# Kernel tuning notes

Measured on AMD Instinct MI355X. Metric: run time of the kernel, lower is better.

The kernel has to match this reference:

```python
import jax, jax.numpy as jnp
import numpy as np

B, T, C, H = 1, 1024, 2048, 32
N = C // H  # head_dim = 64
EPS_GN = 0.00064


def setup_inputs() -> dict:
    key = jax.random.key(0)
    ks = jax.random.split(key, 40)
    f32 = jnp.float32

    def rn(k, shape, s):
        return jax.random.normal(k, shape, f32) * s

    layer_idx, n_layer = 12, 24
    r01 = layer_idx / (n_layer - 1)
    r1a0 = 1.0 - layer_idx / n_layer
    ddd = (jnp.arange(C, dtype=f32) / C).reshape(1, 1, C)
    decay_speed = -7.0 + 5.0 * (jnp.arange(C, dtype=f32) / (C - 1)) ** (0.85 + r01 ** 0.5)

    inp = dict(
        hidden_states=jax.random.normal(ks[0], (B, T, C), f32),
        Wq=rn(ks[1], (C, C), 0.02), Wk=rn(ks[2], (C, C), 0.02),
        Wv=rn(ks[3], (C, C), 0.02), Wo=rn(ks[4], (C, C), 0.02),
        time_maa_x=1.0 - ddd ** (0.6 * r1a0 ** 0.9),
        time_maa_rg=rn(ks[5], (1, 1, C), 0.01),
        time_maa_wa=rn(ks[6], (1, 1, C), 0.01),
        time_maa_k=rn(ks[7], (1, 1, C), 0.01),
        time_maa_v=rn(ks[8], (1, 1, C), 0.01),
        time_maa_w1=rn(ks[9], (C, 4 * 32), 0.01),
        time_maa_w2=rn(ks[10], (4, 32, C), 0.01),
        time_decay=decay_speed.reshape(1, 1, C) + 0.5,
        time_decay_w1=rn(ks[11], (C, 64), 0.01),
        time_decay_w2=rn(ks[12], (64, C), 0.01),
        time_aaaaa=rn(ks[13], (1, 1, C), 0.01),
        time_aaa_w1=rn(ks[14], (C, 16), 0.01),
        time_aaa_w2=rn(ks[15], (16, C), 0.01),
        time_kkk_w1=rn(ks[16], (C, 16), 0.01),
        time_kkk_w2=rn(ks[17], (16, C), 0.01),
        gate_w1=rn(ks[18], (C, 128), 0.01),
        gate_w2=rn(ks[19], (128, C), 0.01),
        time_misc_a=rn(ks[20], (1, 1, C), 0.01),
        ma_w1=rn(ks[21], (C, 16), 0.01),
        ma_w2=rn(ks[22], (16, C), 0.01),
        time_misc_k=rn(ks[23], (1, 1, C), 0.01),
        mk_w1=rn(ks[24], (C, 16), 0.01),
        mk_w2=rn(ks[25], (16, C), 0.01),
        time_faaaa=rn(ks[26], (1, 1, H, N), 0.01),
        ln_w=1.0 + rn(ks[27], (C,), 0.01),
        ln_b=rn(ks[28], (C,), 0.01),
    )
    return inp


def _wkv7(r, w, k, v, a, b):
    """RWKV7 matrix-state recurrence. Inputs [B,T,C]; per head state [N,N].
    state_t = state * exp(w_t) (per key-col) + (state @ a_t) b_t^T + v_t k_t^T;
    out_t = state_t @ r_t."""
    hs = lambda x: x.reshape(B, T, H, N)
    r, k, v, a, b = map(hs, (r, k, v, a, b))
    dec = jnp.exp(hs(w))  # w <= -0.5, decay in (0,1)

    def step(state, inp):
        r_t, d_t, k_t, v_t, a_t, b_t = inp  # each [B,H,N]
        sa = jnp.einsum('bhij,bhj->bhi', state, a_t)
        state = (state * d_t[:, :, None, :]
                 + sa[..., None] * b_t[:, :, None, :]
                 + v_t[..., None] * k_t[:, :, None, :])
        out = jnp.einsum('bhij,bhj->bhi', state, r_t)
        return state, out

    xs = tuple(jnp.moveaxis(t, 1, 0) for t in (r, dec, k, v, a, b))  # [T,B,H,N]
    state0 = jnp.zeros((B, H, N, N), r.dtype)
    _, out = jax.lax.scan(step, state0, xs)
    return jnp.moveaxis(out, 0, 1).reshape(B, T, C)


def _group_norm(x, w, b):
    xg = x.reshape(B, T, H, N)
    mu = xg.mean(-1, keepdims=True)
    var = xg.var(-1, keepdims=True)
    xn = (xg - mu) * jax.lax.rsqrt(var + EPS_GN)
    return xn.reshape(B, T, C) * w + b


def reference(hidden_states, Wq, Wk, Wv, Wo, time_maa_x, time_maa_rg, time_maa_wa,
              time_maa_k, time_maa_v, time_maa_w1, time_maa_w2, time_decay,
              time_decay_w1, time_decay_w2, time_aaaaa, time_aaa_w1, time_aaa_w2,
              time_kkk_w1, time_kkk_w2, gate_w1, gate_w2, time_misc_a, ma_w1, ma_w2,
              time_misc_k, mk_w1, mk_w2, time_faaaa, ln_w, ln_b):
    x = hidden_states  # T already multiple of 16, so no padding branch
    dxprev = jnp.pad(x, ((0, 0), (1, 0), (0, 0)))[:, :-1] - x  # token shift
    xxx = x + dxprev * time_maa_x
    mix = jnp.tanh(xxx @ time_maa_w1).reshape(B, T, 4, 32)
    mix = jnp.einsum('btfd,fdc->fbtc', mix, time_maa_w2)  # [4,B,T,C]
    mrg, mwa, mk_mix, mv = mix[0], mix[1], mix[2], mix[3]
    xrg = x + dxprev * (time_maa_rg + mrg)
    xwa = x + dxprev * (time_maa_wa + mwa)
    xk = x + dxprev * (time_maa_k + mk_mix)
    xv = x + dxprev * (time_maa_v + mv)

    r = xrg @ Wq
    w = -jax.nn.softplus(-(time_decay + jnp.tanh(xwa @ time_decay_w1) @ time_decay_w2)) - 0.5
    k = xk @ Wk
    v = xv @ Wv
    g = jnp.tanh(xrg @ gate_w1) @ gate_w2

    kk = k + jnp.tanh(xk @ time_kkk_w1) @ time_kkk_w2
    kkh = kk.reshape(B, T, H, N)
    kk = (kkh / jnp.maximum(jnp.linalg.norm(kkh, axis=-1, keepdims=True), 1e-12)).reshape(B, T, C)

    a = jax.nn.sigmoid(time_aaaaa + (xwa @ time_aaa_w1) @ time_aaa_w2)
    ma = jax.nn.sigmoid(time_misc_a + (xwa @ ma_w1) @ ma_w2)
    k = k * ma + k * a * (1.0 - ma)
    mk_g = jax.nn.sigmoid(time_misc_k + (xk @ mk_w1) @ mk_w2)
    k = k * jnp.exp(jnp.minimum(w * mk_g, 0.0))

    y = _wkv7(r, w, k, v, -kk, kk * a)
    y = _group_norm(y, ln_w, ln_b)
    rh, kh, vh = (t.reshape(B, T, H, N) for t in (r, k, v))
    y = y + ((rh * kh * time_faaaa).sum(-1, keepdims=True) * vh).reshape(B, T, C)
    return (y * g) @ Wo
```

## Files before the change

### kernel.cpp

```cpp
#include <hip/hip_runtime.h>


#define T_ 1024
#define C_ 2048
#define H_ 32
#define N_ 64

using half8  = __attribute__((ext_vector_type(8))) _Float16;
using half4  = __attribute__((ext_vector_type(4))) _Float16;
using floatx4 = __attribute__((ext_vector_type(4))) float;

#define DPP_ADD(v, ctrl) \
    ((v) + __int_as_float(__builtin_amdgcn_update_dpp( \
        0, __float_as_int(v), (ctrl), 0xf, 0xf, true)))
#define REDUCE16(v) do { \
    v = DPP_ADD(v, 0xB1); v = DPP_ADD(v, 0x4E); \
    v = DPP_ADD(v, 0x141); v = DPP_ADD(v, 0x140); } while (0)

__device__ __forceinline__ void async_cp16(const void* g, void* l) {
    __builtin_amdgcn_global_load_lds(
        (const __attribute__((address_space(1))) void*)g,
        (__attribute__((address_space(3))) void*)l, 16, 0, 0);
}

__global__ __launch_bounds__(256) void k_tr(
    const float* __restrict__ W0, const float* __restrict__ W1,
    const float* __restrict__ W2, const float* __restrict__ W3,
    _Float16* __restrict__ D0, _Float16* __restrict__ D1,
    _Float16* __restrict__ D2, _Float16* __restrict__ D3)
{
    const int z = blockIdx.z;
    const float* S = (z == 0) ? W0 : (z == 1) ? W1 : (z == 2) ? W2 : W3;
    _Float16* D = (z == 0) ? D0 : (z == 1) ? D1 : (z == 2) ? D2 : D3;
    const int nb = blockIdx.x * 64, kb = blockIdx.y * 64;
    __shared__ __align__(16) float tile[64][65];
    const int tr = threadIdx.x >> 4, tc4 = (threadIdx.x & 15) * 4;
#pragma unroll
    for (int p = 0; p < 4; ++p) {
        int row = p * 16 + tr;
        float4 v = *(const float4*)&S[(size_t)(kb + row) * C_ + nb + tc4];
        tile[row][tc4 + 0] = v.x; tile[row][tc4 + 1] = v.y;
        tile[row][tc4 + 2] = v.z; tile[row][tc4 + 3] = v.w;
    }
    __syncthreads();
#pragma unroll
    for (int p = 0; p < 4; ++p) {
        int n = p * 16 + tr;
        half4 u;
        u[0] = (_Float16)tile[tc4 + 0][n];
        u[1] = (_Float16)tile[tc4 + 1][n];
        u[2] = (_Float16)tile[tc4 + 2][n];
        u[3] = (_Float16)tile[tc4 + 3][n];
        *(half4*)&D[(size_t)(nb + n) * C_ + kb + tc4] = u;
    }
}

__global__ __launch_bounds__(256) void k_trW(
    const float* __restrict__ maa_w1, const float* __restrict__ gate_w1,
    const float* __restrict__ decay_w1, const float* __restrict__ aaa_w1,
    const float* __restrict__ ma_w1, const float* __restrict__ kkk_w1,
    const float* __restrict__ mk_w1,
    _Float16* __restrict__ WTm, _Float16* __restrict__ WTl)
{
    const int z = blockIdx.z;
    const int k = blockIdx.x * 256 + threadIdx.x;
    const int n = blockIdx.y;
    if (z == 0 && n >= 128) return;
    const float* src; int stride, col;
    _Float16* dst;
    if (z == 0) { src = maa_w1; stride = 128; col = n; dst = WTm; }
    else {
        dst = WTl;
        if (n < 128)      { src = gate_w1;  stride = 128; col = n; }
        else if (n < 192) { src = decay_w1; stride = 64;  col = n - 128; }
        else if (n < 208) { src = aaa_w1;   stride = 16;  col = n - 192; }
        else if (n < 224) { src = ma_w1;    stride = 16;  col = n - 208; }
        else if (n < 240) { src = kkk_w1;   stride = 16;  col = n - 224; }
        else              { src = mk_w1;    stride = 16;  col = n - 240; }
    }
    dst[(size_t)n * C_ + k] = (_Float16)src[(size_t)k * stride + col];
}

__global__ __launch_bounds__(256) void k_prep(
    const float* __restrict__ X, const float* __restrict__ maa_x,
    _Float16* __restrict__ xxxH)
{
    const size_t idx = (size_t)blockIdx.x * 256 + threadIdx.x;
    const int c = (int)(idx & (C_ - 1));
    float cur = X[idx];
    float prev = (idx >= C_) ? X[idx - C_] : 0.0f;
    xxxH[idx] = (_Float16)(cur + (prev - cur) * maa_x[c]);
}

__global__ __launch_bounds__(256) void k_lora(
    int which,
    const _Float16* __restrict__ Axxx, const _Float16* __restrict__ Axrg,
    const _Float16* __restrict__ Axwa, const _Float16* __restrict__ Axk,
    const _Float16* __restrict__ WTm, const _Float16* __restrict__ WTl,
    float* __restrict__ m1p, float* __restrict__ l2p)
{
    const int mt = blockIdx.x;
    const int nt = blockIdx.y;
    const int ks = blockIdx.z;
    const _Float16* A; const _Float16* BT; float* O; int ostride;
    if (which == 0) { A = Axxx; BT = WTm; O = m1p; ostride = 128; }
    else {
        BT = WTl; O = l2p; ostride = 256;
        A = (nt < 4) ? Axrg : (nt < 7) ? Axwa : Axk;
    }
    O += (size_t)ks * T_ * ostride;
    const int m0 = mt * 64, n0 = nt * 32, k0 = ks * 512;
    const int tid = threadIdx.x;
    __shared__ __align__(16) _Float16 As[64 * 40];
    __shared__ __align__(16) _Float16 Bs[32 * 40];
    const int lane = tid & 63, wv = tid >> 6;
    const int r16 = lane & 15, q = lane >> 4;

    floatx4 acc[2];
    { floatx4 zv = {0.f, 0.f, 0.f, 0.f}; acc[0] = zv; acc[1] = zv; }

    const int arow = tid >> 2, ac8 = (tid & 3) * 8;
    const _Float16* ag = A + (size_t)(m0 + arow) * C_ + k0 + ac8;
    const _Float16* bg = BT + (size_t)(n0 + (tid >> 2)) * C_ + k0 + ac8;

    for (int kc = 0; kc < 512; kc += 32) {
        half8 av = *(const half8*)(ag + kc);
        half8 bv;
        if (tid < 128) bv = *(const half8*)(bg + kc);
        *(half8*)&As[arow * 40 + ac8] = av;
        if (tid < 128) *(half8*)&Bs[(tid >> 2) * 40 + ac8] = bv;
        __syncthreads();
        half8 af = *(const half8*)&As[(wv * 16 + r16) * 40 + q * 8];
        half8 b0 = *(const half8*)&Bs[(r16) * 40 + q * 8];
        half8 b1 = *(const half8*)&Bs[(16 + r16) * 40 + q * 8];
        acc[0] = __builtin_amdgcn_mfma_f32_16x16x32_f16(af, b0, acc[0], 0, 0, 0);
        acc[1] = __builtin_amdgcn_mfma_f32_16x16x32_f16(af, b1, acc[1], 0, 0, 0);
        __syncthreads();
    }
#pragma unroll
    for (int j = 0; j < 2; ++j)
#pragma unroll
        for (int e = 0; e < 4; ++e) {
            int row = m0 + wv * 16 + q * 4 + e;
            int col = n0 + j * 16 + r16;
            O[(size_t)row * ostride + col] = acc[j][e];
        }
}

__global__ __launch_bounds__(256) void k_xmix(
    const float* __restrict__ X, const float* __restrict__ m1p,
    const float* __restrict__ w2,
    const float* __restrict__ mrg, const float* __restrict__ mwa,
    const float* __restrict__ mk, const float* __restrict__ mv,
    _Float16* __restrict__ xrgH, _Float16* __restrict__ xwaH,
    _Float16* __restrict__ xkH, _Float16* __restrict__ xvH)
{
    const int tid = threadIdx.x;
    const int c = blockIdx.x * 256 + tid;
    const int t0 = blockIdx.y * 16;
    const size_t P = (size_t)T_ * 128;
    __shared__ __align__(16) float m1s[16][128];
#pragma unroll
    for (int p = 0; p < 2; ++p) {
        int id = tid + p * 256;
        int r = id >> 5, c4 = (id & 31) * 4;
        size_t off = (size_t)(t0 + r) * 128 + c4;
        float4 v0 = *(const float4*)&m1p[off];
        float4 v1 = *(const float4*)&m1p[P + off];
        float4 v2 = *(const float4*)&m1p[2 * P + off];
        float4 v3 = *(const float4*)&m1p[3 * P + off];
        float4 v;
        v.x = tanhf(((v0.x + v1.x) + v2.x) + v3.x);
        v.y = tanhf(((v0.y + v1.y) + v2.y) + v3.y);
        v.z = tanhf(((v0.z + v1.z) + v2.z) + v3.z);
        v.w = tanhf(((v0.w + v1.w) + v2.w) + v3.w);
        *(float4*)&m1s[r][c4] = v;
    }
    __syncthreads();
    float a0[16], a1[16], a2[16], a3[16];
#pragma unroll
    for (int t = 0; t < 16; ++t) { a0[t] = 0.f; a1[t] = 0.f; a2[t] = 0.f; a3[t] = 0.f; }
    for (int d = 0; d < 32; ++d) {
        float w0 = w2[(size_t)(0 * 32 + d) * C_ + c];
        float w1 = w2[(size_t)(1 * 32 + d) * C_ + c];
        float w2v = w2[(size_t)(2 * 32 + d) * C_ + c];
        float w3 = w2[(size_t)(3 * 32 + d) * C_ + c];
#pragma unroll
        for (int t = 0; t < 16; ++t) {
            a0[t] = fmaf(m1s[t][d],      w0,  a0[t]);
            a1[t] = fmaf(m1s[t][32 + d], w1,  a1[t]);
            a2[t] = fmaf(m1s[t][64 + d], w2v, a2[t]);
            a3[t] = fmaf(m1s[t][96 + d], w3,  a3[t]);
        }
    }
    float vrg = mrg[c], vwa = mwa[c], vmk = mk[c], vmv = mv[c];
    float prev = (t0 > 0) ? X[(size_t)(t0 - 1) * C_ + c] : 0.0f;
    for (int t = 0; t < 16; ++t) {
        size_t idx = (size_t)(t0 + t) * C_ + c;
        float cur = X[idx];
        float dx = prev - cur;
        xrgH[idx] = (_Float16)(cur + dx * (vrg + a0[t]));
        xwaH[idx] = (_Float16)(cur + dx * (vwa + a1[t]));
        xkH[idx]  = (_Float16)(cur + dx * (vmk + a2[t]));
        xvH[idx]  = (_Float16)(cur + dx * (vmv + a3[t]));
        prev = cur;
    }
}

__global__ __launch_bounds__(256) void k_gemm(
    const _Float16* __restrict__ A0, const _Float16* __restrict__ B0, float* __restrict__ C0,
    const _Float16* __restrict__ A1, const _Float16* __restrict__ B1, float* __restrict__ C1,
    const _Float16* __restrict__ A2, const _Float16* __restrict__ B2, float* __restrict__ C2)
{
    const int z = blockIdx.z;
    const _Float16* A = (z == 0) ? A0 : (z == 1) ? A1 : A2;
    const _Float16* Bt = (z == 0) ? B0 : (z == 1) ? B1 : B2;
    float* C = (z == 0) ? C0 : (z == 1) ? C1 : C2;
    const int mtile = blockIdx.y * 128;
    const int ntile = blockIdx.x * 128;
    const int tid = threadIdx.x;
    __shared__ __align__(16) _Float16 As[2][128 * 32];
    __shared__ __align__(16) _Float16 Bs[2][128 * 32];
    const int lane = tid & 63;
    const int wvid = tid >> 6;
    const int wm = wvid >> 1, wn = wvid & 1;
    const int r16 = lane & 15, q = lane >> 4;

    floatx4 acc[4][4];
#pragma unroll
    for (int i = 0; i < 4; ++i)
#pragma unroll
        for (int j = 0; j < 4; ++j) { floatx4 zv = {0.f, 0.f, 0.f, 0.f}; acc[i][j] = zv; }

    const int srow = tid >> 2, sq = tid & 3;
    const _Float16* agA = A + (size_t)(mtile + srow) * C_ + sq * 8;
    const _Float16* agB = Bt + (size_t)(ntile + srow) * C_ + sq * 8;
    const int ldso = srow * 32 + sq * 8;
    const size_t rowoff = (size_t)64 * C_;

    async_cp16(agA, &As[0][ldso]);
    async_cp16(agA + rowoff, &As[0][ldso + 64 * 32]);
    async_cp16(agB, &Bs[0][ldso]);
    async_cp16(agB + rowoff, &Bs[0][ldso + 64 * 32]);

    for (int kc = 0; kc < C_; kc += 32) {
        const int p = (kc >> 5) & 1;
        __syncthreads();
        if (kc + 32 < C_) {
            async_cp16(agA + kc + 32, &As[p ^ 1][ldso]);
            async_cp16(agA + kc + 32 + rowoff, &As[p ^ 1][ldso + 64 * 32]);
            async_cp16(agB + kc + 32, &Bs[p ^ 1][ldso]);
            async_cp16(agB + kc + 32 + rowoff, &Bs[p ^ 1][ldso + 64 * 32]);
        }
        half8 af[4], bf[4];
#pragma unroll
        for (int i = 0; i < 4; ++i)
            af[i] = *(const half8*)&As[p][(wm * 64 + i * 16 + r16) * 32 + q * 8];
#pragma unroll
        for (int j = 0; j < 4; ++j)
            bf[j] = *(const half8*)&Bs[p][(wn * 64 + j * 16 + r16) * 32 + q * 8];
#pragma unroll
        for (int i = 0; i < 4; ++i)
#pragma unroll
            for (int j = 0; j < 4; ++j)
                acc[i][j] = __builtin_amdgcn_mfma_f32_16x16x32_f16(af[i], bf[j], acc[i][j], 0, 0, 0);
    }
#pragma unroll
    for (int i = 0; i < 4; ++i)
#pragma unroll
        for (int j = 0; j < 4; ++j)
#pragma unroll
            for (int e = 0; e < 4; ++e) {
                int row = mtile + wm * 64 + i * 16 + q * 4 + e;
                int col = ntile + wn * 64 + j * 16 + r16;
                C[(size_t)row * C_ + col] = acc[i][j][e];
            }
}

__global__ __launch_bounds__(256) void k_fuse(
    const float* __restrict__ l2p,
    float* __restrict__ K0,
    const float* __restrict__ decay_w2, const float* __restrict__ aaa_w2,
    const float* __restrict__ ma_w2, const float* __restrict__ kkk_w2,
    const float* __restrict__ mk_w2,
    const float* __restrict__ tdecay, const float* __restrict__ aaaaa,
    const float* __restrict__ misc_a, const float* __restrict__ misc_k,
    float* __restrict__ Dout, float* __restrict__ KKout, float* __restrict__ Bout)
{
    const int tid = threadIdx.x;
    const int c = blockIdx.x * 256 + tid;
    const int t0 = blockIdx.y * 16;
    const size_t P = (size_t)T_ * 256;
    __shared__ __align__(16) float wsS[16][96];
    __shared__ __align__(16) float ksS[16][32];
    for (int id = tid; id < 16 * 24; id += 256) {
        int r = id / 24, c4 = (id % 24) * 4;
        size_t off = (size_t)(t0 + r) * 256 + 128 + c4;
        float4 v0 = *(const float4*)&l2p[off];
        float4 v1 = *(const float4*)&l2p[P + off];
        float4 v2 = *(const float4*)&l2p[2 * P + off];
        float4 v3 = *(const float4*)&l2p[3 * P + off];
        float4 v;
        v.x = ((v0.x + v1.x) + v2.x) + v3.x;
        v.y = ((v0.y + v1.y) + v2.y) + v3.y;
        v.z = ((v0.z + v1.z) + v2.z) + v3.z;
        v.w = ((v0.w + v1.w) + v2.w) + v3.w;
        if (c4 < 64) { v.x = tanhf(v.x); v.y = tanhf(v.y); v.z = tanhf(v.z); v.w = tanhf(v.w); }
        *(float4*)&wsS[r][c4] = v;
    }
    for (int id = tid; id < 16 * 8; id += 256) {
        int r = id / 8, c4 = (id % 8) * 4;
        size_t off = (size_t)(t0 + r) * 256 + 224 + c4;
        float4 v0 = *(const float4*)&l2p[off];
        float4 v1 = *(const float4*)&l2p[P + off];
        float4 v2 = *(const float4*)&l2p[2 * P + off];
        float4 v3 = *(const float4*)&l2p[3 * P + off];
        float4 v;
        v.x = ((v0.x + v1.x) + v2.x) + v3.x;
        v.y = ((v0.y + v1.y) + v2.y) + v3.y;
        v.z = ((v0.z + v1.z) + v2.z) + v3.z;
        v.w = ((v0.w + v1.w) + v2.w) + v3.w;
        if (c4 < 16) { v.x = tanhf(v.x); v.y = tanhf(v.y); v.z = tanhf(v.z); v.w = tanhf(v.w); }
        *(float4*)&ksS[r][c4] = v;
    }
    __syncthreads();
    float accW[16], accA[16], accMA[16], accKK[16], accMK[16];
#pragma unroll
    for (int r = 0; r < 16; ++r) { accW[r] = 0.f; accA[r] = 0.f; accMA[r] = 0.f; accKK[r] = 0.f; accMK[r] = 0.f; }
    for (int j = 0; j < 64; ++j) {
        float w = decay_w2[(size_t)j * C_ + c];
#pragma unroll
        for (int r = 0; r < 16; ++r) accW[r] = fmaf(wsS[r][j], w, accW[r]);
    }
    for (int j = 0; j < 16; ++j) {
        float wa = aaa_w2[(size_t)j * C_ + c];
        float wm = ma_w2[(size_t)j * C_ + c];
        float wk = kkk_w2[(size_t)j * C_ + c];
        float wq = mk_w2[(size_t)j * C_ + c];
#pragma unroll
        for (int r = 0; r < 16; ++r) {
            accA[r]  = fmaf(wsS[r][64 + j], wa, accA[r]);
            accMA[r] = fmaf(wsS[r][80 + j], wm, accMA[r]);
            accKK[r] = fmaf(ksS[r][j],      wk, accKK[r]);
            accMK[r] = fmaf(ksS[r][16 + j], wq, accMK[r]);
        }
    }
    float td = tdecay[c], aa = aaaaa[c], mia = misc_a[c], mik = misc_k[c];
    for (int r = 0; r < 16; ++r) {
        size_t idx = (size_t)(t0 + r) * C_ + c;
        float wraw = td + accW[r];
        float w = -logf(1.0f + __expf(-wraw)) - 0.5f;
        float a  = 1.0f / (1.0f + __expf(-(aa  + accA[r])));
        float mav = 1.0f / (1.0f + __expf(-(mia + accMA[r])));
        float mkv = 1.0f / (1.0f + __expf(-(mik + accMK[r])));
        float k0 = K0[idx];
        float kkun = k0 + accKK[r];
        float ss = kkun * kkun;
        REDUCE16(ss);
        ss += __shfl_xor(ss, 16, 64);
        ss += __shfl_xor(ss, 32, 64);
        float kn = kkun * (1.0f / fmaxf(sqrtf(ss), 1e-12f));
        Dout[idx]  = __expf(w);
        KKout[idx] = kn;
        Bout[idx]  = kn * a;
        K0[idx]    = k0 * (mav + a * (1.0f - mav)) * __expf(fminf(w * mkv, 0.0f));
    }
}

__global__ __launch_bounds__(256) void k_wkv(
    const float* __restrict__ R, const float* __restrict__ DEC,
    const float* __restrict__ K, const float* __restrict__ V,
    const float* __restrict__ KK, const float* __restrict__ Bb,
    float* __restrict__ Y)
{
    const int tid = threadIdx.x;
    const int h = blockIdx.x >> 2;
    const int rg = blockIdx.x & 3;
    const int c0 = h * 64;
    const int wv = tid >> 6, lane = tid & 63;
    const int irow = rg * 16 + wv * 4 + (lane >> 4);
    const int jg = lane & 15, j4 = jg * 4;

    __shared__ __align__(16) float rS[2][16][64], dS[2][16][64], kS[2][16][64],
                                   aS[2][16][64], bS[2][16][64];
    __shared__ __align__(16) float vS[2][16][16];

    const int tloc = wv * 4 + (lane >> 4);
    const int sj = (lane & 15) * 4;
    const int vrow = tid >> 2, vc4 = (tid & 3) * 4;

    {
        size_t g = (size_t)tloc * C_ + c0 + sj;
        async_cp16(&R[g],   &rS[0][tloc][sj]);
        async_cp16(&DEC[g], &dS[0][tloc][sj]);
        async_cp16(&K[g],   &kS[0][tloc][sj]);
        async_cp16(&KK[g],  &aS[0][tloc][sj]);
        async_cp16(&Bb[g],  &bS[0][tloc][sj]);
        if (wv == 0)
            async_cp16(&V[(size_t)vrow * C_ + c0 + rg * 16 + vc4], &vS[0][vrow][vc4]);
    }

    float4 s = make_float4(0.f, 0.f, 0.f, 0.f);

    for (int tc = 0; tc < T_; tc += 16) {
        const int p = (tc >> 4) & 1;
        __syncthreads();
        if (tc + 16 < T_) {
            size_t g = (size_t)(tc + 16 + tloc) * C_ + c0 + sj;
            async_cp16(&R[g],   &rS[p ^ 1][tloc][sj]);
            async_cp16(&DEC[g], &dS[p ^ 1][tloc][sj]);
            async_cp16(&K[g],   &kS[p ^ 1][tloc][sj]);
            async_cp16(&KK[g],  &aS[p ^ 1][tloc][sj]);
            async_cp16(&Bb[g],  &bS[p ^ 1][tloc][sj]);
            if (wv == 0)
                async_cp16(&V[(size_t)(tc + 16 + vrow) * C_ + c0 + rg * 16 + vc4],
                           &vS[p ^ 1][vrow][vc4]);
        }
#pragma unroll
        for (int tt = 0; tt < 16; ++tt) {
            float4 kk = *(float4*)&aS[p][tt][j4];
            float sa = -(s.x * kk.x + s.y * kk.y + s.z * kk.z + s.w * kk.w);
            REDUCE16(sa);
            float4 d = *(float4*)&dS[p][tt][j4];
            float4 b = *(float4*)&bS[p][tt][j4];
            float4 k = *(float4*)&kS[p][tt][j4];
            float vi = vS[p][tt][wv * 4 + (lane >> 4)];
            s.x = fmaf(s.x, d.x, fmaf(sa, b.x, vi * k.x));
            s.y = fmaf(s.y, d.y, fmaf(sa, b.y, vi * k.y));
            s.z = fmaf(s.z, d.z, fmaf(sa, b.z, vi * k.z));
            s.w = fmaf(s.w, d.w, fmaf(sa, b.w, vi * k.w));
            float4 r = *(float4*)&rS[p][tt][j4];
            float o = s.x * r.x + s.y * r.y + s.z * r.z + s.w * r.w;
            REDUCE16(o);
            if (jg == 0) Y[(size_t)(tc + tt) * C_ + c0 + irow] = o;
        }
    }
}

__global__ __launch_bounds__(256) void k_gn(
    const float* __restrict__ Y, const float* __restrict__ R, const float* __restrict__ K,
    const float* __restrict__ V, const float* __restrict__ l2p,
    const float* __restrict__ gw2,
    const float* __restrict__ faaaa, const float* __restrict__ lnw,
    const float* __restrict__ lnb, _Float16* __restrict__ YG)
{
    const int t = blockIdx.y;
    const int c = blockIdx.x * 256 + threadIdx.x;
    const size_t idx = (size_t)t * C_ + c;
    __shared__ __align__(16) float gs[128];
    if (threadIdx.x < 128) {
        const size_t P = (size_t)T_ * 256;
        size_t off = (size_t)t * 256 + threadIdx.x;
        float v = ((l2p[off] + l2p[P + off]) + l2p[2 * P + off]) + l2p[3 * P + off];
        gs[threadIdx.x] = tanhf(v);
    }
    __syncthreads();
    float y = Y[idx];
    float s1 = y, s2 = y * y;
#pragma unroll
    for (int off = 1; off < 64; off <<= 1) {
        s1 += __shfl_xor(s1, off, 64);
        s2 += __shfl_xor(s2, off, 64);
    }
    float mu = s1 * (1.0f / 64.0f);
    float var = s2 * (1.0f / 64.0f) - mu * mu;
    float gn = (y - mu) * rsqrtf(var + 0.00064f) * lnw[c] + lnb[c];
    float p = R[idx] * K[idx] * faaaa[c];
#pragma unroll
    for (int off = 1; off < 64; off <<= 1) p += __shfl_xor(p, off, 64);
    float y2 = gn + p * V[idx];
    float g = 0.f;
    for (int j = 0; j < 128; ++j) g = fmaf(gs[j], gw2[(size_t)j * C_ + c], g);
    YG[idx] = (_Float16)(y2 * g);
}

extern "C" void kernel_launch(void* const* d_in, const int* in_sizes, int n_in,
                              void* d_out, int out_size, void* d_ws, size_t ws_size,
                              hipStream_t stream)
{
    (void)in_sizes; (void)n_in; (void)out_size; (void)ws_size;
    const float* hidden   = (const float*)d_in[0];
    const float* Wq       = (const float*)d_in[1];
    const float* Wk       = (const float*)d_in[2];
    const float* Wv       = (const float*)d_in[3];
    const float* Wo       = (const float*)d_in[4];
    const float* maa_x    = (const float*)d_in[5];
    const float* maa_rg   = (const float*)d_in[6];
    const float* maa_wa   = (const float*)d_in[7];
    const float* maa_k    = (const float*)d_in[8];
    const float* maa_v    = (const float*)d_in[9];
    const float* maa_w1   = (const float*)d_in[10];
    const float* maa_w2   = (const float*)d_in[11];
    const float* tdecay   = (const float*)d_in[12];
    const float* decay_w1 = (const float*)d_in[13];
    const float* decay_w2 = (const float*)d_in[14];
    const float* aaaaa    = (const float*)d_in[15];
    const float* aaa_w1   = (const float*)d_in[16];
    const float* aaa_w2   = (const float*)d_in[17];
    const float* kkk_w1   = (const float*)d_in[18];
    const float* kkk_w2   = (const float*)d_in[19];
    const float* gate_w1  = (const float*)d_in[20];
    const float* gate_w2  = (const float*)d_in[21];
    const float* misc_a   = (const float*)d_in[22];
    const float* ma_w1    = (const float*)d_in[23];
    const float* ma_w2    = (const float*)d_in[24];
    const float* misc_k   = (const float*)d_in[25];
    const float* mk_w1    = (const float*)d_in[26];
    const float* mk_w2    = (const float*)d_in[27];
    const float* faaaa    = (const float*)d_in[28];
    const float* lnw      = (const float*)d_in[29];
    const float* lnb      = (const float*)d_in[30];

    float* ws = (float*)d_ws;
    const size_t TC = (size_t)T_ * C_;
    float* S0 = ws + 0 * TC;
    float* S2 = ws + 2 * TC;
    float* S3 = ws + 3 * TC;
    float* S4 = ws + 4 * TC;
    float* S5 = ws + 5 * TC;
    float* S6 = ws + 6 * TC;
    float* S7 = ws + 7 * TC;
    float* m1p = ws + 8 * TC;
    float* l2p = m1p + (size_t)4 * T_ * 128;
    _Float16* WTq = (_Float16*)(l2p + (size_t)4 * T_ * 256);
    _Float16* WTk = WTq + (size_t)C_ * C_;
    _Float16* WTv = WTk + (size_t)C_ * C_;
    _Float16* WTo = WTv + (size_t)C_ * C_;
    _Float16* WTm = WTo + (size_t)C_ * C_;
    _Float16* WTl = WTm + (size_t)128 * C_;
    _Float16* xxxH = WTl + (size_t)256 * C_;
    _Float16* xrgH = xxxH + TC;
    _Float16* xwaH = xrgH + TC;
    _Float16* xkH  = xwaH + TC;
    _Float16* xvH  = xkH + TC;
    _Float16* ygH  = xxxH;
    float* out = (float*)d_out;

    k_tr<<<dim3(32, 32, 4), 256, 0, stream>>>(Wq, Wk, Wv, Wo, WTq, WTk, WTv, WTo);
    k_trW<<<dim3(8, 256, 2), 256, 0, stream>>>(maa_w1, gate_w1, decay_w1,
        aaa_w1, ma_w1, kkk_w1, mk_w1, WTm, WTl);
    k_prep<<<dim3((int)(TC / 256)), 256, 0, stream>>>(hidden, maa_x, xxxH);
    k_lora<<<dim3(16, 4, 4), 256, 0, stream>>>(0, xxxH, xxxH, xxxH, xxxH,
        WTm, WTl, m1p, l2p);
    k_xmix<<<dim3(8, 64), 256, 0, stream>>>(hidden, m1p, maa_w2,
        maa_rg, maa_wa, maa_k, maa_v, xrgH, xwaH, xkH, xvH);
    k_lora<<<dim3(16, 8, 4), 256, 0, stream>>>(1, xxxH, xrgH, xwaH, xkH,
        WTm, WTl, m1p, l2p);
    k_gemm<<<dim3(16, 8, 3), 256, 0, stream>>>(
        xrgH, WTq, S4,  xkH, WTk, S6,  xvH, WTv, S7);
    k_fuse<<<dim3(8, 64), 256, 0, stream>>>(l2p, S6, decay_w2, aaa_w2, ma_w2,
        kkk_w2, mk_w2, tdecay, aaaaa, misc_a, misc_k, S5, S3, S2);
    k_wkv<<<dim3(128), 256, 0, stream>>>(S4, S5, S6, S7, S3, S2, S0);
    k_gn<<<dim3(8, 1024), 256, 0, stream>>>(S0, S4, S6, S7, l2p, gate_w2,
        faaaa, lnw, lnb, ygH);
    k_gemm<<<dim3(16, 8, 1), 256, 0, stream>>>(
        ygH, WTo, out,  ygH, WTo, out,  ygH, WTo, out);
}
```

Baseline: 605.9 us.

## Split WKV across more blocks with register prefetch; batch gate rows in group-norm kernel

The WKV recurrence kernel now runs 256 blocks of 128 threads, each handling 8 state rows instead of 16, so more CUs take part in the serial scan. Within each step the next step's shared-memory operands are prefetched into registers, taking LDS latency off the dependent chain. The group-norm/gate kernel now handles 16 timesteps per block, so each gate_w2 weight load is reused across 16 rows instead of being reread for every timestep. The trade-off is more redundant staging of r/k/decay tiles across WKV blocks and higher register pressure in both kernels.

Result: no change. 599.9 us (-1.0%).

```diff
diff --git a/kernel.cpp b/kernel.cpp
--- a/kernel.cpp
+++ b/kernel.cpp
@@ -367,74 +367,87 @@
     }
 }
 
-__global__ __launch_bounds__(256) void k_wkv(
+__global__ __launch_bounds__(128) void k_wkv(
     const float* __restrict__ R, const float* __restrict__ DEC,
     const float* __restrict__ K, const float* __restrict__ V,
     const float* __restrict__ KK, const float* __restrict__ Bb,
     float* __restrict__ Y)
 {
     const int tid = threadIdx.x;
-    const int h = blockIdx.x >> 2;
-    const int rg = blockIdx.x & 3;
+    const int h = blockIdx.x >> 3;
+    const int rg = blockIdx.x & 7;
     const int c0 = h * 64;
     const int wv = tid >> 6, lane = tid & 63;
-    const int irow = rg * 16 + wv * 4 + (lane >> 4);
+    const int rowslot = lane >> 4;
+    const int lrow = wv * 4 + rowslot;
+    const int irow = rg * 8 + lrow;
     const int jg = lane & 15, j4 = jg * 4;
 
     __shared__ __align__(16) float rS[2][16][64], dS[2][16][64], kS[2][16][64],
                                    aS[2][16][64], bS[2][16][64];
-    __shared__ __align__(16) float vS[2][16][16];
-
-    const int tloc = wv * 4 + (lane >> 4);
-    const int sj = (lane & 15) * 4;
-    const int vrow = tid >> 2, vc4 = (tid & 3) * 4;
-
-    {
-        size_t g = (size_t)tloc * C_ + c0 + sj;
-        async_cp16(&R[g],   &rS[0][tloc][sj]);
-        async_cp16(&DEC[g], &dS[0][tloc][sj]);
-        async_cp16(&K[g],   &kS[0][tloc][sj]);
-        async_cp16(&KK[g],  &aS[0][tloc][sj]);
-        async_cp16(&Bb[g],  &bS[0][tloc][sj]);
-        if (wv == 0)
-            async_cp16(&V[(size_t)vrow * C_ + c0 + rg * 16 + vc4], &vS[0][vrow][vc4]);
-    }
+    __shared__ __align__(16) float vS[2][16][8];
+
+    const int s0_step = tid >> 4, s0_q4 = (tid & 15) * 4;
+    const int s1_step = (tid + 128) >> 4, s1_q4 = ((tid + 128) & 15) * 4;
+    const int v_step = tid >> 1, v_q4 = (tid & 1) * 4;
+
+#define WKV_STAGE(buf, tcb) do {                                              \
+    size_t g0 = (size_t)((tcb) + s0_step) * C_ + c0 + s0_q4;                  \
+    size_t g1 = (size_t)((tcb) + s1_step) * C_ + c0 + s1_q4;                  \
+    async_cp16(&R[g0],   &rS[buf][s0_step][s0_q4]);                           \
+    async_cp16(&R[g1],   &rS[buf][s1_step][s1_q4]);                           \
+    async_cp16(&DEC[g0], &dS[buf][s0_step][s0_q4]);                           \
+    async_cp16(&DEC[g1], &dS[buf][s1_step][s1_q4]);                           \
+    async_cp16(&K[g0],   &kS[buf][s0_step][s0_q4]);                           \
+    async_cp16(&K[g1],   &kS[buf][s1_step][s1_q4]);                           \
+    async_cp16(&KK[g0],  &aS[buf][s0_step][s0_q4]);                           \
+    async_cp16(&KK[g1],  &aS[buf][s1_step][s1_q4]);                           \
+    async_cp16(&Bb[g0],  &bS[buf][s0_step][s0_q4]);                           \
+    async_cp16(&Bb[g1],  &bS[buf][s1_step][s1_q4]);                           \
+    if (tid < 32)                                                             \
+        async_cp16(&V[(size_t)((tcb) + v_step) * C_ + c0 + rg * 8 + v_q4],    \
+                   &vS[buf][v_step][v_q4]);                                   \
+} while (0)
+
+    WKV_STAGE(0, 0);
 
     float4 s = make_float4(0.f, 0.f, 0.f, 0.f);
 
     for (int tc = 0; tc < T_; tc += 16) {
         const int p = (tc >> 4) & 1;
         __syncthreads();
-        if (tc + 16 < T_) {
-            size_t g = (size_t)(tc + 16 + tloc) * C_ + c0 + sj;
-            async_cp16(&R[g],   &rS[p ^ 1][tloc][sj]);
-            async_cp16(&DEC[g], &dS[p ^ 1][tloc][sj]);
-            async_cp16(&K[g],   &kS[p ^ 1][tloc][sj]);
-            async_cp16(&KK[g],  &aS[p ^ 1][tloc][sj]);
-            async_cp16(&Bb[g],  &bS[p ^ 1][tloc][sj]);
-            if (wv == 0)
-                async_cp16(&V[(size_t)(tc + 16 + vrow) * C_ + c0 + rg * 16 + vc4],
-                           &vS[p ^ 1][vrow][vc4]);
-        }
+        if (tc + 16 < T_) WKV_STAGE(p ^ 1, tc + 16);
+
+        float4 cr = *(float4*)&rS[p][0][j4];
+        float4 cd = *(float4*)&dS[p][0][j4];
+        float4 ck = *(float4*)&kS[p][0][j4];
+        float4 ca = *(float4*)&aS[p][0][j4];
+        float4 cb = *(float4*)&bS[p][0][j4];
+        float   cv = vS[p][0][lrow];
 #pragma unroll
         for (int tt = 0; tt < 16; ++tt) {
-            float4 kk = *(float4*)&aS[p][tt][j4];
-            float sa = -(s.x * kk.x + s.y * kk.y + s.z * kk.z + s.w * kk.w);
+            float4 nr, nd, nk, na, nb; float nv = 0.f;
+            if (tt < 15) {
+                nr = *(float4*)&rS[p][tt + 1][j4];
+                nd = *(float4*)&dS[p][tt + 1][j4];
+                nk = *(float4*)&kS[p][tt + 1][j4];
+                na = *(float4*)&aS[p][tt + 1][j4];
+                nb = *(float4*)&bS[p][tt + 1][j4];
+                nv = vS[p][tt + 1][lrow];
+            }
+            float sa = -(s.x * ca.x + s.y * ca.y + s.z * ca.z + s.w * ca.w);
             REDUCE16(sa);
-            float4 d = *(float4*)&dS[p][tt][j4];
-            float4 b = *(float4*)&bS[p][tt][j4];
-            float4 k = *(float4*)&kS[p][tt][j4];
-            float vi = vS[p][tt][wv * 4 + (lane >> 4)];
-            s.x = fmaf(s.x, d.x, fmaf(sa, b.x, vi * k.x));
-            s.y = fmaf(s.y, d.y, fmaf(sa, b.y, vi * k.y));
-            s.z = fmaf(s.z, d.z, fmaf(sa, b.z, vi * k.z));
-            s.w = fmaf(s.w, d.w, fmaf(sa, b.w, vi * k.w));
-            float4 r = *(float4*)&rS[p][tt][j4];
-            float o = s.x * r.x + s.y * r.y + s.z * r.z + s.w * r.w;
+            s.x = fmaf(s.x, cd.x, fmaf(sa, cb.x, cv * ck.x));
+            s.y = fmaf(s.y, cd.y, fmaf(sa, cb.y, cv * ck.y));
+            s.z = fmaf(s.z, cd.z, fmaf(sa, cb.z, cv * ck.z));
+            s.w = fmaf(s.w, cd.w, fmaf(sa, cb.w, cv * ck.w));
+            float o = s.x * cr.x + s.y * cr.y + s.z * cr.z + s.w * cr.w;
             REDUCE16(o);
             if (jg == 0) Y[(size_t)(tc + tt) * C_ + c0 + irow] = o;
+            cr = nr; cd = nd; ck = nk; ca = na; cb = nb; cv = nv;
         }
     }
+#undef WKV_STAGE
 }
 
 __global__ __launch_bounds__(256) void k_gn(
@@ -444,34 +457,45 @@
     const float* __restrict__ faaaa, const float* __restrict__ lnw,
     const float* __restrict__ lnb, _Float16* __restrict__ YG)
 {
-    const int t = blockIdx.y;
-    const int c = blockIdx.x * 256 + threadIdx.x;
-    const size_t idx = (size_t)t * C_ + c;
-    __shared__ __align__(16) float gs[128];
-    if (threadIdx.x < 128) {
-        const size_t P = (size_t)T_ * 256;
-        size_t off = (size_t)t * 256 + threadIdx.x;
+    const int tid = threadIdx.x;
+    const int c = blockIdx.x * 256 + tid;
+    const int t0 = blockIdx.y * 16;
+    const size_t P = (size_t)T_ * 256;
+    __shared__ __align__(16) float gs[16][128];
+    for (int id = tid; id < 16 * 128; id += 256) {
+        int r = id >> 7, cc = id & 127;
+        size_t off = (size_t)(t0 + r) * 256 + cc;
         float v = ((l2p[off] + l2p[P + off]) + l2p[2 * P + off]) + l2p[3 * P + off];
-        gs[threadIdx.x] = tanhf(v);
+        gs[r][cc] = tanhf(v);
     }
     __syncthreads();
-    float y = Y[idx];
-    float s1 = y, s2 = y * y;
-#pragma unroll
-    for (int off = 1; off < 64; off <<= 1) {
-        s1 += __shfl_xor(s1, off, 64);
-        s2 += __shfl_xor(s2, off, 64);
-    }
-    float mu = s1 * (1.0f / 64.0f);
-    float var = s2 * (1.0f / 64.0f) - mu * mu;
-    float gn = (y - mu) * rsqrtf(var + 0.00064f) * lnw[c] + lnb[c];
-    float p = R[idx] * K[idx] * faaaa[c];
-#pragma unroll
-    for (int off = 1; off < 64; off <<= 1) p += __shfl_xor(p, off, 64);
-    float y2 = gn + p * V[idx];
-    float g = 0.f;
-    for (int j = 0; j < 128; ++j) g = fmaf(gs[j], gw2[(size_t)j * C_ + c], g);
-    YG[idx] = (_Float16)(y2 * g);
+    float gacc[16];
+#pragma unroll
+    for (int r = 0; r < 16; ++r) gacc[r] = 0.f;
+    for (int j = 0; j < 128; ++j) {
+        float w = gw2[(size_t)j * C_ + c];
+#pragma unroll
+        for (int r = 0; r < 16; ++r) gacc[r] = fmaf(gs[r][j], w, gacc[r]);
+    }
+    float fa = faaaa[c], lw = lnw[c], lb = lnb[c];
+    for (int r = 0; r < 16; ++r) {
+        const size_t idx = (size_t)(t0 + r) * C_ + c;
+        float y = Y[idx];
+        float s1 = y, s2 = y * y;
+#pragma unroll
+        for (int off = 1; off < 64; off <<= 1) {
+            s1 += __shfl_xor(s1, off, 64);
+            s2 += __shfl_xor(s2, off, 64);
+        }
+        float mu = s1 * (1.0f / 64.0f);
+        float var = s2 * (1.0f / 64.0f) - mu * mu;
+        float gn = (y - mu) * rsqrtf(var + 0.00064f) * lw + lb;
+        float p = R[idx] * K[idx] * fa;
+#pragma unroll
+        for (int off = 1; off < 64; off <<= 1) p += __shfl_xor(p, off, 64);
+        float y2 = gn + p * V[idx];
+        YG[idx] = (_Float16)(y2 * gacc[r]);
+    }
 }
 
 extern "C" void kernel_launch(void* const* d_in, const int* in_sizes, int n_in,
@@ -550,8 +574,8 @@
         xrgH, WTq, S4,  xkH, WTk, S6,  xvH, WTv, S7);
     k_fuse<<<dim3(8, 64), 256, 0, stream>>>(l2p, S6, decay_w2, aaa_w2, ma_w2,
         kkk_w2, mk_w2, tdecay, aaaaa, misc_a, misc_k, S5, S3, S2);
-    k_wkv<<<dim3(128), 256, 0, stream>>>(S4, S5, S6, S7, S3, S2, S0);
-    k_gn<<<dim3(8, 1024), 256, 0, stream>>>(S0, S4, S6, S7, l2p, gate_w2,
+    k_wkv<<<dim3(256), 128, 0, stream>>>(S4, S5, S6, S7, S3, S2, S0);
+    k_gn<<<dim3(8, 64), 256, 0, stream>>>(S0, S4, S6, S7, l2p, gate_w2,
         faaaa, lnw, lnb, ygH);
     k_gemm<<<dim3(16, 8, 1), 256, 0, stream>>>(
         ygH, WTo, out,  ygH, WTo, out,  ygH, WTo, out);
```
